# Kernel optimization log

Hardware: AMD Instinct MI355X
Metric: run time of the kernel (lower is better)

## Reference

```python
import jax, jax.numpy as jnp
import numpy as np

B, S, H = 8, 2048, 512

def setup_inputs() -> dict:
    key = jax.random.key(0)
    k1, k2, k3 = jax.random.split(key, 3)
    # scale inputs down so unstabilized exp(Q.x) stays finite (module has no softmax max-subtract)
    input_data = jax.random.normal(k1, (B, S, H), dtype=jnp.float32) * 0.05
    W = jax.random.normal(k2, (H, H), dtype=jnp.float32) * (1.0 / np.sqrt(H))
    b = jax.random.normal(k3, (H,), dtype=jnp.float32) * 0.01
    return {"input_data": input_data, "W": W, "b": b}

def reference(input_data, W, b):
    # Q[b,i,:] = Linear(input_data[b,i,:])  -- the 'correlated value'
    q = jnp.einsum('bsh,oh->bso', input_data, W) + b            # [B,S,H]
    # score[b,i,j] = exp( Q_i . x_j )   (no max-subtraction, faithful to original)
    scores = jnp.exp(jnp.einsum('bih,bjh->bij', q, input_data))  # [B,S,S]
    # strictly-causal mask: triu(ones,1).T == lower-triangular with zero diagonal (j < i)
    mask = jnp.tril(jnp.ones((S, S), dtype=input_data.dtype), k=-1)
    masked = scores * mask                                       # [B,S,S]
    denom = jnp.sum(masked, axis=-1, keepdims=True) + 1e-10      # [B,S,1]
    attn = masked / denom                                        # [B,S,S]
    # weighted sum of raw inputs over past positions j
    out = jnp.einsum('bij,bjh->bih', attn, input_data)           # [B,S,H]
    return out
```

## Files before the change

kernel.cpp:

```cpp
#include <hip/hip_runtime.h>
#include <hip/hip_bf16.h>

#define BATCH 8
#define SEQ   2048
#define DIM   512

typedef __bf16 bf16x8 __attribute__((ext_vector_type(8)));
typedef float  f32x4  __attribute__((ext_vector_type(4)));

__device__ __forceinline__ ushort f2bf(float f) {
    union { float f; unsigned u; } c; c.f = f;
    unsigned u = c.u;
    u += 0x7fffu + ((u >> 16) & 1u);
    return (ushort)(u >> 16);
}

__global__ __launch_bounds__(256) void prep_kernel(const float* __restrict__ X,
                                                   ushort* __restrict__ Xb,
                                                   ushort* __restrict__ Xt,
                                                   const float* __restrict__ W,
                                                   ushort* __restrict__ Wb) {
    __shared__ ushort T[32 * 33];
    int t   = threadIdx.x;
    int bid = blockIdx.x;
    if (bid >= 8192) {
        int gt = (bid - 8192) * 256 + t;
        size_t base = (size_t)gt * 8;
        float4 a = *(const float4*)(W + base);
        float4 c = *(const float4*)(W + base + 4);
        ushort4 lo, hi;
        lo.x = f2bf(a.x); lo.y = f2bf(a.y); lo.z = f2bf(a.z); lo.w = f2bf(a.w);
        hi.x = f2bf(c.x); hi.y = f2bf(c.y); hi.z = f2bf(c.z); hi.w = f2bf(c.w);
        *(ushort4*)(Wb + base)     = lo;
        *(ushort4*)(Wb + base + 4) = hi;
        return;
    }
    int b   = bid >> 10;
    int st  = (bid >> 4) & 63;
    int ht  = bid & 15;
    int s0 = st * 32, h0 = ht * 32;

    int r  = t >> 3;
    int c4 = (t & 7) * 4;
    size_t src = ((size_t)(b * SEQ + s0 + r)) * DIM + h0 + c4;
    float4 v = *(const float4*)(X + src);
    ushort u0 = f2bf(v.x), u1 = f2bf(v.y), u2 = f2bf(v.z), u3 = f2bf(v.w);
    ushort4 uv; uv.x = u0; uv.y = u1; uv.z = u2; uv.w = u3;
    *(ushort4*)(Xb + src) = uv;
    T[(c4 + 0) * 33 + r] = u0;
    T[(c4 + 1) * 33 + r] = u1;
    T[(c4 + 2) * 33 + r] = u2;
    T[(c4 + 3) * 33 + r] = u3;
    __syncthreads();
    int hh = t >> 3;
    int sc = (t & 7) * 4;
    ushort4 w;
    w.x = T[hh * 33 + sc + 0];
    w.y = T[hh * 33 + sc + 1];
    w.z = T[hh * 33 + sc + 2];
    w.w = T[hh * 33 + sc + 3];
    *(ushort4*)(Xt + ((size_t)(b * DIM + h0 + hh)) * SEQ + s0 + sc) = w;
}

__global__ __launch_bounds__(256, 2) void qgemm_kernel(const ushort* __restrict__ Xb,
                                                       const ushort* __restrict__ Wb,
                                                       const float* __restrict__ bias,
                                                       ushort* __restrict__ Qb) {
    __shared__ ushort At[2][128 * 72];
    __shared__ ushort Bt[2][128 * 72];
    int t   = threadIdx.x;
    int bid = blockIdx.x;
    int mt = bid >> 2, nt = bid & 3;
    int m0 = mt << 7, n0 = nt << 7;
    int w  = t >> 6, l = t & 63, ln = l & 15, lg = l >> 4;
    int wr = w >> 1, wc = w & 1;

    f32x4 acc[4][4] = {};
    int arow = t >> 1;
    int ac0  = (t & 1) * 32;

    const ushort* Arow = Xb + (size_t)m0 * 512;
    const ushort* Brow = Wb + (size_t)n0 * 512;

#define QG_LOAD(KS, A0, A1, A2, A3, B0, B1, B2, B3)                                \
    {                                                                              \
        const ushort* pa_ = Arow + (size_t)arow * 512 + (KS) * 64 + ac0;           \
        A0 = *(const uint4*)(pa_ + 0);  A1 = *(const uint4*)(pa_ + 8);             \
        A2 = *(const uint4*)(pa_ + 16); A3 = *(const uint4*)(pa_ + 24);            \
        const ushort* pb_ = Brow + (size_t)arow * 512 + (KS) * 64 + ac0;           \
        B0 = *(const uint4*)(pb_ + 0);  B1 = *(const uint4*)(pb_ + 8);             \
        B2 = *(const uint4*)(pb_ + 16); B3 = *(const uint4*)(pb_ + 24);            \
    }

#define QG_STORE(CUR, A0, A1, A2, A3, B0, B1, B2, B3)            \
    {                                                            \
        ushort* la_ = &At[CUR][arow * 72 + ac0];                 \
        *(uint4*)(la_ + 0) = A0;  *(uint4*)(la_ + 8) = A1;       \
        *(uint4*)(la_ + 16) = A2; *(uint4*)(la_ + 24) = A3;      \
        ushort* lb_ = &Bt[CUR][arow * 72 + ac0];                 \
        *(uint4*)(lb_ + 0) = B0;  *(uint4*)(lb_ + 8) = B1;       \
        *(uint4*)(lb_ + 16) = B2; *(uint4*)(lb_ + 24) = B3;      \
    }

#define QG_COMPUTE(CUR)                                                                      \
    {                                                                                        \
        _Pragma("unroll") for (int kk = 0; kk < 2; ++kk) {                                   \
            bf16x8 af[4], bfr[4];                                                            \
            _Pragma("unroll") for (int r = 0; r < 4; ++r)                                    \
                af[r] = *(const bf16x8*)&At[CUR][(wr * 64 + r * 16 + ln) * 72 + kk * 32 + lg * 8]; \
            _Pragma("unroll") for (int cc = 0; cc < 4; ++cc)                                 \
                bfr[cc] = *(const bf16x8*)&Bt[CUR][(wc * 64 + cc * 16 + ln) * 72 + kk * 32 + lg * 8]; \
            _Pragma("unroll") for (int r = 0; r < 4; ++r)                                    \
                _Pragma("unroll") for (int cc = 0; cc < 4; ++cc)                             \
                    acc[r][cc] = __builtin_amdgcn_mfma_f32_16x16x32_bf16(af[r], bfr[cc],     \
                                                                         acc[r][cc], 0, 0, 0); \
        }                                                                                    \
    }

    uint4 pA0, pA1, pA2, pA3, pB0, pB1, pB2, pB3;
    uint4 qA0, qA1, qA2, qA3, qB0, qB1, qB2, qB3;
    QG_LOAD(0, pA0, pA1, pA2, pA3, pB0, pB1, pB2, pB3)
    QG_LOAD(1, qA0, qA1, qA2, qA3, qB0, qB1, qB2, qB3)
    QG_STORE(0, pA0, pA1, pA2, pA3, pB0, pB1, pB2, pB3)
    __syncthreads();
    for (int ks = 0; ks < 6; ks += 2) {
        QG_LOAD(ks + 2, pA0, pA1, pA2, pA3, pB0, pB1, pB2, pB3)
        QG_COMPUTE(0)
        QG_STORE(1, qA0, qA1, qA2, qA3, qB0, qB1, qB2, qB3)
        __syncthreads();
        QG_LOAD(ks + 3, qA0, qA1, qA2, qA3, qB0, qB1, qB2, qB3)
        QG_COMPUTE(1)
        QG_STORE(0, pA0, pA1, pA2, pA3, pB0, pB1, pB2, pB3)
        __syncthreads();
    }
    QG_COMPUTE(0)
    QG_STORE(1, qA0, qA1, qA2, qA3, qB0, qB1, qB2, qB3)
    __syncthreads();
    QG_COMPUTE(1)

    float bv[4];
#pragma unroll
    for (int c = 0; c < 4; ++c) bv[c] = bias[n0 + wc * 64 + c * 16 + ln];
#pragma unroll
    for (int r = 0; r < 4; ++r)
#pragma unroll
        for (int c = 0; c < 4; ++c)
#pragma unroll
            for (int q = 0; q < 4; ++q) {
                int row = m0 + wr * 64 + r * 16 + lg * 4 + q;
                int col = n0 + wc * 64 + c * 16 + ln;
                Qb[(size_t)row * 512 + col] = f2bf(acc[r][c][q] + bv[c]);
            }
}

__global__ __launch_bounds__(256, 3) void sgemm_kernel(const ushort* __restrict__ Qb,
                                                       const ushort* __restrict__ Xb,
                                                       ushort* __restrict__ Pb,
                                                       int g0, int G) {
    __shared__ ushort SMEM[20480];
#define SG_AT(C) (SMEM + (C) * 5120)
#define SG_BT(C) (SMEM + 10240 + (C) * 5120)
    int t  = threadIdx.x;
    int bL = blockIdx.x;
    int b  = g0 + bL;
    int c  = blockIdx.y;
    int it = 0, base = 0;
    for (;;) { if (c < base + it + 1) break; base += it + 1; ++it; }
    int jt = c - base;

    int m0 = it << 7, n0 = jt << 7;
    int w  = t >> 6, l = t & 63, ln = l & 15, lg = l >> 4;
    int wr = w >> 1, wc = w & 1;

    const ushort* Arow = Qb + (size_t)(b * SEQ + m0) * 512;
    const ushort* Brow = Xb + (size_t)(b * SEQ + n0) * 512;

    f32x4 acc[4][4] = {};
    int srow = t >> 2;
    int sc8  = (t & 3) * 8;

#define SG_LOAD(KS, A0, A1, B0, B1)                                                \
    A0 = *(const uint4*)(Arow + (size_t)srow * 512 + (KS) * 32 + sc8);             \
    A1 = *(const uint4*)(Arow + (size_t)(64 + srow) * 512 + (KS) * 32 + sc8);      \
    B0 = *(const uint4*)(Brow + (size_t)srow * 512 + (KS) * 32 + sc8);             \
    B1 = *(const uint4*)(Brow + (size_t)(64 + srow) * 512 + (KS) * 32 + sc8);

#define SG_STORE(CUR, A0, A1, B0, B1)                       \
    {                                                       \
        *(uint4*)&SG_AT(CUR)[srow * 40 + sc8]        = A0;  \
        *(uint4*)&SG_AT(CUR)[(64 + srow) * 40 + sc8] = A1;  \
        *(uint4*)&SG_BT(CUR)[srow * 40 + sc8]        = B0;  \
        *(uint4*)&SG_BT(CUR)[(64 + srow) * 40 + sc8] = B1;  \
    }

#define SG_COMPUTE(CUR)                                                                    \
    {                                                                                      \
        bf16x8 af[4], bfr[4];                                                              \
        _Pragma("unroll") for (int r = 0; r < 4; ++r)                                      \
            af[r] = *(const bf16x8*)&SG_AT(CUR)[(wr * 64 + r * 16 + ln) * 40 + lg * 8];    \
        _Pragma("unroll") for (int cc = 0; cc < 4; ++cc)                                   \
            bfr[cc] = *(const bf16x8*)&SG_BT(CUR)[(wc * 64 + cc * 16 + ln) * 40 + lg * 8]; \
        _Pragma("unroll") for (int r = 0; r < 4; ++r)                                      \
            _Pragma("unroll") for (int cc = 0; cc < 4; ++cc)                               \
                acc[r][cc] = __builtin_amdgcn_mfma_f32_16x16x32_bf16(af[r], bfr[cc],       \
                                                                     acc[r][cc], 0, 0, 0); \
    }

    uint4 pA0, pA1, pB0, pB1, qA0, qA1, qB0, qB1;
    SG_LOAD(0, pA0, pA1, pB0, pB1)
    SG_LOAD(1, qA0, qA1, qB0, qB1)
    SG_STORE(0, pA0, pA1, pB0, pB1)
    __syncthreads();
    for (int ks = 0; ks < 14; ks += 2) {
        SG_LOAD(ks + 2, pA0, pA1, pB0, pB1)
        SG_COMPUTE(0)
        SG_STORE(1, qA0, qA1, qB0, qB1)
        __syncthreads();
        SG_LOAD(ks + 3, qA0, qA1, qB0, qB1)
        SG_COMPUTE(1)
        SG_STORE(0, pA0, pA1, pB0, pB1)
        __syncthreads();
    }
    SG_COMPUTE(0)
    SG_STORE(1, qA0, qA1, qB0, qB1)
    __syncthreads();
    SG_COMPUTE(1)
    __syncthreads();

#pragma unroll
    for (int r = 0; r < 4; ++r)
#pragma unroll
        for (int q = 0; q < 4; ++q) {
            int prow = wr * 64 + r * 16 + lg * 4 + q;
            int grow = m0 + prow;
#pragma unroll
            for (int cc = 0; cc < 4; ++cc) {
                int pcol = wc * 64 + cc * 16 + ln;
                int col  = n0 + pcol;
                float ex = (col < grow) ? __expf(acc[r][cc][q]) : 0.f;
                SMEM[prow * 128 + pcol] = f2bf(ex);
            }
        }
    __syncthreads();

    ushort* ptile = Pb + ((size_t)c * G + bL) * 16384;
#pragma unroll
    for (int k2 = 0; k2 < 8; ++k2)
        *(uint4*)(ptile + k2 * 2048 + t * 8) = *(const uint4*)(SMEM + k2 * 2048 + t * 8);
}

__global__ __launch_bounds__(256, 2) void pvgemm_kernel(const ushort* __restrict__ Pb,
                                                        const ushort* __restrict__ Xt,
                                                        float* __restrict__ out,
                                                        int g0, int G) {
    __shared__ ushort Ap[2][128 * 72];
    __shared__ ushort Bp[2][64 * 72];
    __shared__ float  dden[128];
    int t  = threadIdx.x;
    int bL = blockIdx.x;
    int b  = g0 + bL;
    int y  = blockIdx.y;
    int p  = y >> 3;
    int ht = y & 7;
    int n0 = ht << 6;

    int w = t >> 6, l = t & 63, ln = l & 15, lg = l >> 4;
    int wr = w >> 1, wc = w & 1;
    int arow = t >> 1;
    int ac0  = (t & 1) * 32;
    int brow = t >> 2;
    int bc0  = (t & 3) * 16;

    const ushort* BrowX = Xt + ((size_t)b * DIM + n0) * SEQ;

    bf16x8 vones;
#pragma unroll
    for (int e = 0; e < 8; ++e) vones[e] = (__bf16)1.0f;

#define PV_LOAD(S, A0, A1, A2, A3, B0, B1)                                              \
    {                                                                                   \
        const ushort* pt_ = Pb + ((size_t)(Tit + ((S) >> 1)) * G + bL) * 16384          \
                            + ((S) & 1) * 64 + (size_t)arow * 128 + ac0;                \
        A0 = *(const uint4*)(pt_ + 0);  A1 = *(const uint4*)(pt_ + 8);                  \
        A2 = *(const uint4*)(pt_ + 16); A3 = *(const uint4*)(pt_ + 24);                 \
        const ushort* pb_ = BrowX + (size_t)brow * 2048 + (S) * 64 + bc0;               \
        B0 = *(const uint4*)(pb_ + 0);  B1 = *(const uint4*)(pb_ + 8);                  \
    }
#define PV_ST(CUR, A0, A1, A2, A3, B0, B1)                       \
    {                                                            \
        ushort* la_ = &Ap[CUR][arow * 72 + ac0];                 \
        *(uint4*)(la_ + 0) = A0;  *(uint4*)(la_ + 8) = A1;       \
        *(uint4*)(la_ + 16) = A2; *(uint4*)(la_ + 24) = A3;      \
        ushort* lb_ = &Bp[CUR][brow * 72 + bc0];                 \
        *(uint4*)(lb_ + 0) = B0;  *(uint4*)(lb_ + 8) = B1;       \
    }
#define PV_COMPUTE(CUR)                                                                     \
    {                                                                                       \
        _Pragma("unroll") for (int kk = 0; kk < 2; ++kk) {                                  \
            bf16x8 af[4], bfr[2];                                                           \
            _Pragma("unroll") for (int r = 0; r < 4; ++r)                                   \
                af[r] = *(const bf16x8*)&Ap[CUR][(wr * 64 + r * 16 + ln) * 72 + kk * 32 + lg * 8]; \
            _Pragma("unroll") for (int cc = 0; cc < 2; ++cc)                                \
                bfr[cc] = *(const bf16x8*)&Bp[CUR][(wc * 32 + cc * 16 + ln) * 72 + kk * 32 + lg * 8]; \
            if (wc == 0) {                                                                  \
                accd0 = __builtin_amdgcn_mfma_f32_16x16x32_bf16(af[0], vones, accd0, 0, 0, 0); \
                accd1 = __builtin_amdgcn_mfma_f32_16x16x32_bf16(af[1], vones, accd1, 0, 0, 0); \
            } else {                                                                        \
                accd0 = __builtin_amdgcn_mfma_f32_16x16x32_bf16(af[2], vones, accd0, 0, 0, 0); \
                accd1 = __builtin_amdgcn_mfma_f32_16x16x32_bf16(af[3], vones, accd1, 0, 0, 0); \
            }                                                                               \
            _Pragma("unroll") for (int r = 0; r < 4; ++r)                                   \
                _Pragma("unroll") for (int cc = 0; cc < 2; ++cc)                            \
                    acc[r][cc] = __builtin_amdgcn_mfma_f32_16x16x32_bf16(af[r], bfr[cc],    \
                                                                         acc[r][cc], 0, 0, 0); \
        }                                                                                   \
    }

    for (int half = 0; half < 2; ++half) {
        int it  = half ? p : (15 - p);
        int Tit = (it * (it + 1)) >> 1;
        int n   = (it + 1) * 2;
        int m0  = it << 7;
        f32x4 acc[4][2] = {};
        f32x4 accd0 = {}, accd1 = {};

        uint4 pA0, pA1, pA2, pA3, pB0, pB1;
        uint4 qA0, qA1, qA2, qA3, qB0, qB1;
        PV_LOAD(0, pA0, pA1, pA2, pA3, pB0, pB1)
        PV_LOAD(1, qA0, qA1, qA2, qA3, qB0, qB1)
        __syncthreads();
        PV_ST(0, pA0, pA1, pA2, pA3, pB0, pB1)
        __syncthreads();
        for (int ks = 0; ks < n - 2; ks += 2) {
            PV_LOAD(ks + 2, pA0, pA1, pA2, pA3, pB0, pB1)
            PV_COMPUTE(0)
            PV_ST(1, qA0, qA1, qA2, qA3, qB0, qB1)
            __syncthreads();
            if (ks + 3 < n) PV_LOAD(ks + 3, qA0, qA1, qA2, qA3, qB0, qB1)
            PV_COMPUTE(1)
            PV_ST(0, pA0, pA1, pA2, pA3, pB0, pB1)
            __syncthreads();
        }
        PV_COMPUTE(0)
        PV_ST(1, qA0, qA1, qA2, qA3, qB0, qB1)
        __syncthreads();
        PV_COMPUTE(1)

        if (ln == 0) {
#pragma unroll
            for (int q = 0; q < 4; ++q) {
                dden[wr * 64 + (wc * 2) * 16 + lg * 4 + q]     = accd0[q];
                dden[wr * 64 + (wc * 2 + 1) * 16 + lg * 4 + q] = accd1[q];
            }
        }
        __syncthreads();

#pragma unroll
        for (int r = 0; r < 4; ++r)
#pragma unroll
            for (int q = 0; q < 4; ++q) {
                int lrow = wr * 64 + r * 16 + lg * 4 + q;
                int row  = m0 + lrow;
                float inv = 1.0f / (dden[lrow] + 1e-10f);
                size_t o = (size_t)(b * SEQ + row) * 512;
#pragma unroll
                for (int cc = 0; cc < 2; ++cc)
                    out[o + n0 + wc * 32 + cc * 16 + ln] = acc[r][cc][q] * inv;
            }
        __syncthreads();
    }
}

extern "C" void kernel_launch(void* const* d_in, const int* in_sizes, int n_in,
                              void* d_out, int out_size, void* d_ws, size_t ws_size,
                              hipStream_t stream) {
    const float* X    = (const float*)d_in[0];
    const float* W    = (const float*)d_in[1];
    const float* bias = (const float*)d_in[2];
    float* out = (float*)d_out;

    ushort* ws = (ushort*)d_ws;
    ushort* Xb = ws;
    ushort* Xt = ws + 8388608;
    ushort* Qb = ws + 16777216;
    ushort* Wb = ws + 25165824;
    ushort* Pb = (ushort*)((char*)d_ws + 50855936);

    size_t avail = (ws_size > 50855936) ? (ws_size - 50855936) : 0;
    int G = 1;
    while (G < 8 && (size_t)(G * 2) * 4456448 <= avail) G *= 2;

    prep_kernel<<<dim3(8320), dim3(256), 0, stream>>>(X, Xb, Xt, W, Wb);
    qgemm_kernel<<<dim3(512), dim3(256), 0, stream>>>(Xb, Wb, bias, Qb);
    for (int g0 = 0; g0 < BATCH; g0 += G) {
        sgemm_kernel<<<dim3(G, 136), dim3(256), 0, stream>>>(Qb, Xb, Pb, g0, G);
        pvgemm_kernel<<<dim3(G, 64), dim3(256), 0, stream>>>(Pb, Xt, out, g0, G);
    }
}
```

Before: 91.92 us.

## Widen PV GEMM column tile to 128 and drop paired row-tile balancing

The PV GEMM block now covers 128 output columns instead of 64, so each loaded P tile is reused across twice as many columns, halving P reads. Each block handles a single row tile, ordered longest first, instead of pairing a long and a short tile. This costs more accumulator registers and LDS and gives less even per-block work.

```diff
diff --git a/kernel.cpp b/kernel.cpp
--- a/kernel.cpp
+++ b/kernel.cpp
@@ -254,22 +254,23 @@
                                                         float* __restrict__ out,
                                                         int g0, int G) {
     __shared__ ushort Ap[2][128 * 72];
-    __shared__ ushort Bp[2][64 * 72];
+    __shared__ ushort Bp[2][128 * 72];
     __shared__ float  dden[128];
     int t  = threadIdx.x;
     int bL = blockIdx.x;
     int b  = g0 + bL;
     int y  = blockIdx.y;
-    int p  = y >> 3;
-    int ht = y & 7;
-    int n0 = ht << 6;
+    int it = 15 - (y >> 2);
+    int ht = y & 3;
+    int n0 = ht << 7;
+    int m0 = it << 7;
+    int Tit = (it * (it + 1)) >> 1;
+    int nks = (it + 1) * 2;
 
     int w = t >> 6, l = t & 63, ln = l & 15, lg = l >> 4;
     int wr = w >> 1, wc = w & 1;
     int arow = t >> 1;
     int ac0  = (t & 1) * 32;
-    int brow = t >> 2;
-    int bc0  = (t & 3) * 16;
 
     const ushort* BrowX = Xt + ((size_t)b * DIM + n0) * SEQ;
 
@@ -277,31 +278,33 @@
 #pragma unroll
     for (int e = 0; e < 8; ++e) vones[e] = (__bf16)1.0f;
 
-#define PV_LOAD(S, A0, A1, A2, A3, B0, B1)                                              \
+#define PV_LOAD(S, A0, A1, A2, A3, B0, B1, B2, B3)                                      \
     {                                                                                   \
         const ushort* pt_ = Pb + ((size_t)(Tit + ((S) >> 1)) * G + bL) * 16384          \
                             + ((S) & 1) * 64 + (size_t)arow * 128 + ac0;                \
         A0 = *(const uint4*)(pt_ + 0);  A1 = *(const uint4*)(pt_ + 8);                  \
         A2 = *(const uint4*)(pt_ + 16); A3 = *(const uint4*)(pt_ + 24);                 \
-        const ushort* pb_ = BrowX + (size_t)brow * 2048 + (S) * 64 + bc0;               \
+        const ushort* pb_ = BrowX + (size_t)arow * 2048 + (S) * 64 + ac0;               \
         B0 = *(const uint4*)(pb_ + 0);  B1 = *(const uint4*)(pb_ + 8);                  \
-    }
-#define PV_ST(CUR, A0, A1, A2, A3, B0, B1)                       \
+        B2 = *(const uint4*)(pb_ + 16); B3 = *(const uint4*)(pb_ + 24);                 \
+    }
+#define PV_ST(CUR, A0, A1, A2, A3, B0, B1, B2, B3)               \
     {                                                            \
         ushort* la_ = &Ap[CUR][arow * 72 + ac0];                 \
         *(uint4*)(la_ + 0) = A0;  *(uint4*)(la_ + 8) = A1;       \
         *(uint4*)(la_ + 16) = A2; *(uint4*)(la_ + 24) = A3;      \
-        ushort* lb_ = &Bp[CUR][brow * 72 + bc0];                 \
+        ushort* lb_ = &Bp[CUR][arow * 72 + ac0];                 \
         *(uint4*)(lb_ + 0) = B0;  *(uint4*)(lb_ + 8) = B1;       \
+        *(uint4*)(lb_ + 16) = B2; *(uint4*)(lb_ + 24) = B3;      \
     }
 #define PV_COMPUTE(CUR)                                                                     \
     {                                                                                       \
         _Pragma("unroll") for (int kk = 0; kk < 2; ++kk) {                                  \
-            bf16x8 af[4], bfr[2];                                                           \
+            bf16x8 af[4], bfr[4];                                                           \
             _Pragma("unroll") for (int r = 0; r < 4; ++r)                                   \
                 af[r] = *(const bf16x8*)&Ap[CUR][(wr * 64 + r * 16 + ln) * 72 + kk * 32 + lg * 8]; \
-            _Pragma("unroll") for (int cc = 0; cc < 2; ++cc)                                \
-                bfr[cc] = *(const bf16x8*)&Bp[CUR][(wc * 32 + cc * 16 + ln) * 72 + kk * 32 + lg * 8]; \
+            _Pragma("unroll") for (int cc = 0; cc < 4; ++cc)                                \
+                bfr[cc] = *(const bf16x8*)&Bp[CUR][(wc * 64 + cc * 16 + ln) * 72 + kk * 32 + lg * 8]; \
             if (wc == 0) {                                                                  \
                 accd0 = __builtin_amdgcn_mfma_f32_16x16x32_bf16(af[0], vones, accd0, 0, 0, 0); \
                 accd1 = __builtin_amdgcn_mfma_f32_16x16x32_bf16(af[1], vones, accd1, 0, 0, 0); \
@@ -310,65 +313,57 @@
                 accd1 = __builtin_amdgcn_mfma_f32_16x16x32_bf16(af[3], vones, accd1, 0, 0, 0); \
             }                                                                               \
             _Pragma("unroll") for (int r = 0; r < 4; ++r)                                   \
-                _Pragma("unroll") for (int cc = 0; cc < 2; ++cc)                            \
+                _Pragma("unroll") for (int cc = 0; cc < 4; ++cc)                            \
                     acc[r][cc] = __builtin_amdgcn_mfma_f32_16x16x32_bf16(af[r], bfr[cc],    \
                                                                          acc[r][cc], 0, 0, 0); \
         }                                                                                   \
     }
 
-    for (int half = 0; half < 2; ++half) {
-        int it  = half ? p : (15 - p);
-        int Tit = (it * (it + 1)) >> 1;
-        int n   = (it + 1) * 2;
-        int m0  = it << 7;
-        f32x4 acc[4][2] = {};
-        f32x4 accd0 = {}, accd1 = {};
-
-        uint4 pA0, pA1, pA2, pA3, pB0, pB1;
-        uint4 qA0, qA1, qA2, qA3, qB0, qB1;
-        PV_LOAD(0, pA0, pA1, pA2, pA3, pB0, pB1)
-        PV_LOAD(1, qA0, qA1, qA2, qA3, qB0, qB1)
-        __syncthreads();
-        PV_ST(0, pA0, pA1, pA2, pA3, pB0, pB1)
-        __syncthreads();
-        for (int ks = 0; ks < n - 2; ks += 2) {
-            PV_LOAD(ks + 2, pA0, pA1, pA2, pA3, pB0, pB1)
-            PV_COMPUTE(0)
-            PV_ST(1, qA0, qA1, qA2, qA3, qB0, qB1)
-            __syncthreads();
-            if (ks + 3 < n) PV_LOAD(ks + 3, qA0, qA1, qA2, qA3, qB0, qB1)
-            PV_COMPUTE(1)
-            PV_ST(0, pA0, pA1, pA2, pA3, pB0, pB1)
-            __syncthreads();
+    f32x4 acc[4][4] = {};
+    f32x4 accd0 = {}, accd1 = {};
+
+    uint4 pA0, pA1, pA2, pA3, pB0, pB1, pB2, pB3;
+    uint4 qA0, qA1, qA2, qA3, qB0, qB1, qB2, qB3;
+    PV_LOAD(0, pA0, pA1, pA2, pA3, pB0, pB1, pB2, pB3)
+    PV_LOAD(1, qA0, qA1, qA2, qA3, qB0, qB1, qB2, qB3)
+    PV_ST(0, pA0, pA1, pA2, pA3, pB0, pB1, pB2, pB3)
+    __syncthreads();
+    for (int ks = 0; ks < nks - 2; ks += 2) {
+        PV_LOAD(ks + 2, pA0, pA1, pA2, pA3, pB0, pB1, pB2, pB3)
+        PV_COMPUTE(0)
+        PV_ST(1, qA0, qA1, qA2, qA3, qB0, qB1, qB2, qB3)
+        __syncthreads();
+        if (ks + 3 < nks) PV_LOAD(ks + 3, qA0, qA1, qA2, qA3, qB0, qB1, qB2, qB3)
+        PV_COMPUTE(1)
+        PV_ST(0, pA0, pA1, pA2, pA3, pB0, pB1, pB2, pB3)
+        __syncthreads();
+    }
+    PV_COMPUTE(0)
+    PV_ST(1, qA0, qA1, qA2, qA3, qB0, qB1, qB2, qB3)
+    __syncthreads();
+    PV_COMPUTE(1)
+
+    if (ln == 0) {
+#pragma unroll
+        for (int q = 0; q < 4; ++q) {
+            dden[wr * 64 + (wc * 2) * 16 + lg * 4 + q]     = accd0[q];
+            dden[wr * 64 + (wc * 2 + 1) * 16 + lg * 4 + q] = accd1[q];
         }
-        PV_COMPUTE(0)
-        PV_ST(1, qA0, qA1, qA2, qA3, qB0, qB1)
-        __syncthreads();
-        PV_COMPUTE(1)
-
-        if (ln == 0) {
-#pragma unroll
-            for (int q = 0; q < 4; ++q) {
-                dden[wr * 64 + (wc * 2) * 16 + lg * 4 + q]     = accd0[q];
-                dden[wr * 64 + (wc * 2 + 1) * 16 + lg * 4 + q] = accd1[q];
-            }
+    }
+    __syncthreads();
+
+#pragma unroll
+    for (int r = 0; r < 4; ++r)
+#pragma unroll
+        for (int q = 0; q < 4; ++q) {
+            int lrow = wr * 64 + r * 16 + lg * 4 + q;
+            int row  = m0 + lrow;
+            float inv = 1.0f / (dden[lrow] + 1e-10f);
+            size_t o = (size_t)(b * SEQ + row) * 512;
+#pragma unroll
+            for (int cc = 0; cc < 4; ++cc)
+                out[o + n0 + wc * 64 + cc * 16 + ln] = acc[r][cc][q] * inv;
         }
-        __syncthreads();
-
-#pragma unroll
-        for (int r = 0; r < 4; ++r)
-#pragma unroll
-            for (int q = 0; q < 4; ++q) {
-                int lrow = wr * 64 + r * 16 + lg * 4 + q;
-                int row  = m0 + lrow;
-                float inv = 1.0f / (dden[lrow] + 1e-10f);
-                size_t o = (size_t)(b * SEQ + row) * 512;
-#pragma unroll
-                for (int cc = 0; cc < 2; ++cc)
-                    out[o + n0 + wc * 32 + cc * 16 + ln] = acc[r][cc][q] * inv;
-            }
-        __syncthreads();
-    }
 }
 
 extern "C" void kernel_launch(void* const* d_in, const int* in_sizes, int n_in,
```

New measurement: 93.75 us. No clear change (+2.0%).
